# Optimization experiments

Hardware: AMD Instinct MI355X
Metric: run time of the kernel (lower is better)

## Reference

```python
import jax, jax.numpy as jnp
import numpy as np

EPS = 1e-5

def _layernorm(x, g, b):
    mu = jnp.mean(x, axis=-1, keepdims=True)
    var = jnp.mean(jnp.square(x - mu), axis=-1, keepdims=True)
    return (x - mu) / jnp.sqrt(var + EPS) * g + b

def setup_inputs() -> dict:
    key = jax.random.key(0)
    ks = jax.random.split(key, 8)
    B, T, E, H, Dh, F = 4, 2048, 1024, 16, 64, 4096
    s = lambda fan: 1.0 / np.sqrt(fan)
    return {
        "x":  jax.random.normal(ks[0], (B, T, E), jnp.float32),
        "Wq": jax.random.normal(ks[1], (H, E, Dh), jnp.float32) * s(E),
        "Wk": jax.random.normal(ks[2], (H, E, Dh), jnp.float32) * s(E),
        "Wv": jax.random.normal(ks[3], (H, E, Dh), jnp.float32) * s(E),
        "Wo": jax.random.normal(ks[4], (E, E), jnp.float32) * s(E),
        "bo": jnp.zeros((E,), jnp.float32),
        "W1": jax.random.normal(ks[5], (E, F), jnp.float32) * s(E),
        "b1": jnp.zeros((F,), jnp.float32),
        "W2": jax.random.normal(ks[6], (F, E), jnp.float32) * s(F),
        "b2": jnp.zeros((E,), jnp.float32),
        "g1": jnp.ones((E,), jnp.float32),
        "bt1": jnp.zeros((E,), jnp.float32),
        "g2": jnp.ones((E,), jnp.float32),
        "bt2": jnp.zeros((E,), jnp.float32),
    }

def reference(x, Wq, Wk, Wv, Wo, bo, W1, b1, W2, b2, g1, bt1, g2, bt2):
    B, T, E = x.shape
    # --- pre-LN multi-head attention (dropout = identity in eval) ---
    h = _layernorm(x, g1, bt1)
    q = jnp.einsum('btc,hcd->bhtd', h, Wq)
    k = jnp.einsum('btc,hcd->bhtd', h, Wk)
    v = jnp.einsum('btc,hcd->bhtd', h, Wv)
    # NOTE: original scales by embed_size**-0.5 (input channel c), not head_size
    scores = jnp.einsum('bhtd,bhsd->bhts', q, k) * (E ** -0.5)
    causal = jnp.tril(jnp.ones((T, T), bool))
    scores = jnp.where(causal, scores, -jnp.inf)
    attn = jax.nn.softmax(scores, axis=-1)
    ctx = jnp.einsum('bhts,bhsd->bhtd', attn, v)
    ctx = ctx.transpose(0, 2, 1, 3).reshape(B, T, E)  # concat heads
    x = x + ctx @ Wo + bo
    # --- pre-LN feed-forward ---
    h2 = _layernorm(x, g2, bt2)
    x = x + jax.nn.relu(h2 @ W1 + b1) @ W2 + b2
    return x
```

## Files before the change

kernel.cpp:

```cpp
#include <hip/hip_runtime.h>

typedef unsigned short u16;
typedef __attribute__((ext_vector_type(8))) short bf16x8;
typedef __attribute__((ext_vector_type(4))) short bf16x4;
typedef __attribute__((ext_vector_type(4))) float f32x4;

#define LOG2E 1.4426950408889634f

__device__ __forceinline__ float b2f(u16 u) {
  union { unsigned int i; float f; } x; x.i = ((unsigned int)u) << 16; return x.f;
}
__device__ __forceinline__ u16 f2b(float f) {
  unsigned int i = __float_as_uint(f);
  unsigned int r = (i + 0x7FFFu + ((i >> 16) & 1u)) >> 16;
  return (u16)r;
}
__device__ __forceinline__ void stc(u16* C, size_t i, float v) { C[i] = f2b(v); }
__device__ __forceinline__ void stc(float* C, size_t i, float v) { C[i] = v; }

__device__ __forceinline__ bool is_f32(const unsigned* probe) {
  return probe[0] == 0x3F800000u;
}
__device__ __forceinline__ float ldin(const void* p, size_t i, bool f32) {
  return f32 ? ((const float*)p)[i] : b2f(((const u16*)p)[i]);
}

__device__ __forceinline__ void gld_lds16(const void* g, void* l) {
  __builtin_amdgcn_global_load_lds(
      (const __attribute__((address_space(1))) unsigned int*)g,
      (__attribute__((address_space(3))) unsigned int*)l, 16, 0, 0);
}

__device__ __forceinline__ void lds_wave_fence() {
  __asm__ volatile("s_waitcnt lgkmcnt(0)" ::: "memory");
}

__device__ __forceinline__ void tr8(unsigned a[4], int lane) {
  unsigned p0, p1, p2, p3;
  p0 = __shfl_xor((int)a[0], 1, 64); p1 = __shfl_xor((int)a[1], 1, 64);
  p2 = __shfl_xor((int)a[2], 1, 64); p3 = __shfl_xor((int)a[3], 1, 64);
  unsigned sel = (lane & 1) ? 0x3276u : 0x5410u;
  a[0] = __byte_perm(a[0], p0, sel); a[1] = __byte_perm(a[1], p1, sel);
  a[2] = __byte_perm(a[2], p2, sel); a[3] = __byte_perm(a[3], p3, sel);
  p0 = __shfl_xor((int)a[0], 2, 64); p1 = __shfl_xor((int)a[1], 2, 64);
  p2 = __shfl_xor((int)a[2], 2, 64); p3 = __shfl_xor((int)a[3], 2, 64);
  if (lane & 2) { a[0] = p1; a[2] = p3; } else { a[1] = p0; a[3] = p2; }
  p0 = __shfl_xor((int)a[0], 4, 64); p1 = __shfl_xor((int)a[1], 4, 64);
  p2 = __shfl_xor((int)a[2], 4, 64); p3 = __shfl_xor((int)a[3], 4, 64);
  if (lane & 4) { a[0] = p2; a[1] = p3; } else { a[2] = p0; a[3] = p1; }
}

__global__ __launch_bounds__(256) void ln_kernel(
    const void* __restrict__ x, int x_raw,
    const void* __restrict__ g, const void* __restrict__ b,
    u16* __restrict__ y, const unsigned* __restrict__ probe) {
  __shared__ float red[4];
  const bool f32 = is_f32(probe);
  int row = blockIdx.x, tid = threadIdx.x;
  int w = tid >> 6;
  float f0, f1, f2, f3;
  if (x_raw && f32) {
    const float* xr = (const float*)x + (size_t)row * 1024 + tid * 4;
    float4 v = *(const float4*)xr;
    f0 = v.x; f1 = v.y; f2 = v.z; f3 = v.w;
  } else {
    const u16* xr = (const u16*)x + (size_t)row * 1024 + tid * 4;
    bf16x4 v = *(const bf16x4*)xr;
    f0 = b2f((u16)v[0]); f1 = b2f((u16)v[1]); f2 = b2f((u16)v[2]); f3 = b2f((u16)v[3]);
  }
  float s = f0 + f1 + f2 + f3;
  #pragma unroll
  for (int o = 32; o >= 1; o >>= 1) s += __shfl_xor(s, o, 64);
  if ((tid & 63) == 0) red[w] = s;
  __syncthreads();
  float mean = (red[0] + red[1] + red[2] + red[3]) * (1.0f / 1024.0f);
  __syncthreads();
  float d0 = f0 - mean, d1 = f1 - mean, d2 = f2 - mean, d3 = f3 - mean;
  float vs = d0 * d0 + d1 * d1 + d2 * d2 + d3 * d3;
  #pragma unroll
  for (int o = 32; o >= 1; o >>= 1) vs += __shfl_xor(vs, o, 64);
  if ((tid & 63) == 0) red[w] = vs;
  __syncthreads();
  float var = (red[0] + red[1] + red[2] + red[3]) * (1.0f / 1024.0f);
  float rstd = rsqrtf(var + 1e-5f);
  int c = tid * 4;
  float o0 = d0 * rstd * ldin(g, c + 0, f32) + ldin(b, c + 0, f32);
  float o1 = d1 * rstd * ldin(g, c + 1, f32) + ldin(b, c + 1, f32);
  float o2 = d2 * rstd * ldin(g, c + 2, f32) + ldin(b, c + 2, f32);
  float o3 = d3 * rstd * ldin(g, c + 3, f32) + ldin(b, c + 3, f32);
  bf16x4 ov; ov[0] = (short)f2b(o0); ov[1] = (short)f2b(o1);
  ov[2] = (short)f2b(o2); ov[3] = (short)f2b(o3);
  *(bf16x4*)(y + (size_t)row * 1024 + c) = ov;
}

__global__ __launch_bounds__(256) void repack_t(
    const void* __restrict__ src, u16* __restrict__ dst, int N, int K,
    const unsigned* __restrict__ probe) {
  const bool f32 = is_f32(probe);
  int flat = blockIdx.x * 256 + threadIdx.x;
  int n = flat % N;
  int c0 = (flat / N) * 8;
  bf16x8 t;
  #pragma unroll
  for (int j = 0; j < 8; j++) t[j] = (short)f2b(ldin(src, (size_t)(c0 + j) * N + n, f32));
  *(bf16x8*)&dst[(size_t)n * K + c0] = t;
}

__global__ __launch_bounds__(256) void repack_qkv(
    const void* __restrict__ Wq, const void* __restrict__ Wk,
    const void* __restrict__ Wv, u16* __restrict__ dst,
    const unsigned* __restrict__ probe) {
  const bool f32 = is_f32(probe);
  int flat = blockIdx.x * 256 + threadIdx.x;
  int n = flat % 3072;
  int c0 = (flat / 3072) * 8;
  const void* W = (n < 1024) ? Wq : (n < 2048) ? Wk : Wv;
  int nn = n & 1023;
  int hn = nn >> 6, d = nn & 63;
  bf16x8 t;
  #pragma unroll
  for (int j = 0; j < 8; j++)
    t[j] = (short)f2b(ldin(W, (size_t)hn * 65536 + (size_t)(c0 + j) * 64 + d, f32));
  *(bf16x8*)&dst[(size_t)n * 1024 + c0] = t;
}

template <int EPI, typename CT>
__global__ __launch_bounds__(256) void gemm_bt(
    const u16* __restrict__ A, const u16* __restrict__ Bt, CT* __restrict__ C,
    int M, int N, int K, const void* __restrict__ bias,
    const void* __restrict__ res, int res_raw,
    const unsigned* __restrict__ probe) {
  __shared__ __align__(16) u16 sA[128 * 32];
  __shared__ __align__(16) u16 sB[128 * 32];
  const bool f32 = is_f32(probe);
  int tid = threadIdx.x;
  int w = tid >> 6, lane = tid & 63;
  int l15 = lane & 15, q4 = lane >> 4;
  int bm = blockIdx.x * 128, bn = blockIdx.y * 128;
  int wm = (w & 1) * 64, wn = (w >> 1) * 64;
  f32x4 acc[4][4] = {};
  for (int k0 = 0; k0 < K; k0 += 32) {
    #pragma unroll
    for (int j = 0; j < 2; ++j) {
      int c = j * 256 + tid;
      int row = c >> 2, ck = (c & 3) * 8;
      gld_lds16(A + (size_t)(bm + row) * K + k0 + ck, &sA[c * 8]);
    }
    #pragma unroll
    for (int j = 0; j < 2; ++j) {
      int c = j * 256 + tid;
      int row = c >> 2, ck = (c & 3) * 8;
      gld_lds16(Bt + (size_t)(bn + row) * K + k0 + ck, &sB[c * 8]);
    }
    __syncthreads();
    bf16x8 af[4], bf[4];
    #pragma unroll
    for (int i = 0; i < 4; i++) af[i] = *(const bf16x8*)&sA[(wm + i * 16 + l15) * 32 + q4 * 8];
    #pragma unroll
    for (int j = 0; j < 4; j++) bf[j] = *(const bf16x8*)&sB[(wn + j * 16 + l15) * 32 + q4 * 8];
    #pragma unroll
    for (int i = 0; i < 4; i++)
      #pragma unroll
      for (int j = 0; j < 4; j++)
        acc[i][j] = __builtin_amdgcn_mfma_f32_16x16x32_bf16(af[i], bf[j], acc[i][j], 0, 0, 0);
    __syncthreads();
  }
  #pragma unroll
  for (int i = 0; i < 4; i++) {
    int rg = bm + wm + i * 16 + q4 * 4;
    #pragma unroll
    for (int j = 0; j < 4; j++) {
      int cg = bn + wn + j * 16 + l15;
      float bv = (EPI > 0) ? ldin(bias, cg, f32) : 0.0f;
      #pragma unroll
      for (int r = 0; r < 4; r++) {
        float v = acc[i][j][r];
        if (EPI == 1) v += bv + ldin(res, (size_t)(rg + r) * N + cg, res_raw && f32);
        if (EPI == 2) { v += bv; v = fmaxf(v, 0.0f); }
        stc(C, (size_t)(rg + r) * N + cg, v);
      }
    }
  }
}

__global__ __launch_bounds__(256) void attn_kernel(
    const u16* __restrict__ qkv, u16* __restrict__ ctx, int T) {
  __shared__ __align__(16) u16 sK[64 * 68];
  __shared__ __align__(16) u16 sVt[64 * 68];
  __shared__ __align__(16) u16 sP[8 * 16 * 68];
  int tid = threadIdx.x;
  int w = tid >> 6, lane = tid & 63;
  int l15 = lane & 15, q4 = lane >> 4;

  int n = blockIdx.x;
  int qi = n & 15;
  int h = (n >> 4) & 15;
  int b = (n >> 8) & 3;
  int qbase = (qi & 1) ? (qi >> 1) : (15 - (qi >> 1));
  int qt = (qbase + 7 * b) & 15;
  int qt0 = qt * 128;
  int mb[2] = {qt0 + w * 16, qt0 + 64 + w * 16};
  size_t b3072 = (size_t)(b * T) * 3072;

  bf16x8 qf[2][2];
  #pragma unroll
  for (int m = 0; m < 2; m++) {
    const u16* qr = qkv + b3072 + (size_t)(mb[m] + l15) * 3072 + h * 64;
    qf[m][0] = *(const bf16x8*)(qr + q4 * 8);
    qf[m][1] = *(const bf16x8*)(qr + 32 + q4 * 8);
  }
  f32x4 o[2][4] = {};
  float mx[2][4], ls[2][4];
  #pragma unroll
  for (int m = 0; m < 2; m++)
    #pragma unroll
    for (int r = 0; r < 4; r++) { mx[m][r] = -1e30f; ls[m][r] = 0.f; }

  int ktmax = 2 * qt + 1;
  for (int kt = 0; kt <= ktmax; ++kt) {
    int s0 = kt * 64;
    bf16x8 kreg[2]; int krow[2], kcol[2];
    #pragma unroll
    for (int j = 0; j < 2; ++j) {
      int c = j * 256 + tid;
      krow[j] = c >> 3; kcol[j] = (c & 7) * 8;
      kreg[j] = *(const bf16x8*)(qkv + b3072 + (size_t)(s0 + krow[j]) * 3072 + 1024 + h * 64 + kcol[j]);
    }
    unsigned va[4], vb[4];
    {
      const u16* vs = qkv + b3072 + (size_t)(s0 + lane) * 3072 + 2048 + h * 64 + w * 16;
      *(bf16x8*)va = *(const bf16x8*)vs;
      *(bf16x8*)vb = *(const bf16x8*)(vs + 8);
    }
    __syncthreads();
    #pragma unroll
    for (int j = 0; j < 2; ++j)
      *(bf16x8*)&sK[krow[j] * 68 + kcol[j]] = kreg[j];
    tr8(va, lane); tr8(vb, lane);
    {
      int dd = w * 16 + (lane & 7), t0 = (lane >> 3) * 8;
      *(bf16x8*)&sVt[dd * 68 + t0] = *(bf16x8*)va;
      *(bf16x8*)&sVt[(dd + 8) * 68 + t0] = *(bf16x8*)vb;
    }
    __syncthreads();

    bool act0 = (s0 <= mb[0] + 15);
    f32x4 s[2][4];
    #pragma unroll
    for (int j = 0; j < 4; ++j) {
      bf16x8 k0 = *(const bf16x8*)&sK[(j * 16 + l15) * 68 + q4 * 8];
      bf16x8 k1 = *(const bf16x8*)&sK[(j * 16 + l15) * 68 + 32 + q4 * 8];
      if (act0) {
        f32x4 z = {0.f, 0.f, 0.f, 0.f};
        z = __builtin_amdgcn_mfma_f32_16x16x32_bf16(qf[0][0], k0, z, 0, 0, 0);
        s[0][j] = __builtin_amdgcn_mfma_f32_16x16x32_bf16(qf[0][1], k1, z, 0, 0, 0);
      }
      f32x4 z = {0.f, 0.f, 0.f, 0.f};
      z = __builtin_amdgcn_mfma_f32_16x16x32_bf16(qf[1][0], k0, z, 0, 0, 0);
      s[1][j] = __builtin_amdgcn_mfma_f32_16x16x32_bf16(qf[1][1], k1, z, 0, 0, 0);
    }
    #pragma unroll
    for (int m = 0; m < 2; ++m) {
      if (m == 0 && !act0) continue;
      int mbm = mb[m];
      if (s0 + 63 > mbm) {
        #pragma unroll
        for (int j = 0; j < 4; ++j)
          #pragma unroll
          for (int r = 0; r < 4; ++r) {
            float v = s[m][j][r] * 0.03125f;
            if (s0 + j * 16 + l15 > mbm + q4 * 4 + r) v = -1e30f;
            s[m][j][r] = v;
          }
      } else {
        #pragma unroll
        for (int j = 0; j < 4; ++j)
          #pragma unroll
          for (int r = 0; r < 4; ++r) s[m][j][r] *= 0.03125f;
      }
      float tm[4];
      #pragma unroll
      for (int r = 0; r < 4; ++r)
        tm[r] = fmaxf(fmaxf(s[m][0][r], s[m][1][r]), fmaxf(s[m][2][r], s[m][3][r]));
      #pragma unroll
      for (int off = 8; off >= 1; off >>= 1)
        #pragma unroll
        for (int r = 0; r < 4; ++r) tm[r] = fmaxf(tm[r], __shfl_xor(tm[r], off, 64));
      float al[4], ts[4];
      #pragma unroll
      for (int r = 0; r < 4; ++r) {
        float mn = fmaxf(mx[m][r], tm[r]);
        al[r] = __builtin_amdgcn_exp2f((mx[m][r] - mn) * LOG2E);
        mx[m][r] = mn; ts[r] = 0.f;
      }
      int pbase = (w * 2 + m) * 1088;
      #pragma unroll
      for (int j = 0; j < 4; ++j)
        #pragma unroll
        for (int r = 0; r < 4; ++r) {
          float p = __builtin_amdgcn_exp2f((s[m][j][r] - mx[m][r]) * LOG2E);
          ts[r] += p;
          sP[pbase + (q4 * 4 + r) * 68 + j * 16 + l15] = f2b(p);
        }
      #pragma unroll
      for (int off = 8; off >= 1; off >>= 1)
        #pragma unroll
        for (int r = 0; r < 4; ++r) ts[r] += __shfl_xor(ts[r], off, 64);
      #pragma unroll
      for (int r = 0; r < 4; ++r) ls[m][r] = ls[m][r] * al[r] + ts[r];
      #pragma unroll
      for (int j = 0; j < 4; ++j)
        #pragma unroll
        for (int r = 0; r < 4; ++r) o[m][j][r] *= al[r];
    }
    lds_wave_fence();
    bf16x8 pf[2][2];
    #pragma unroll
    for (int m = 0; m < 2; ++m) {
      if (m == 0 && !act0) continue;
      int pbase = (w * 2 + m) * 1088;
      pf[m][0] = *(const bf16x8*)&sP[pbase + l15 * 68 + q4 * 8];
      pf[m][1] = *(const bf16x8*)&sP[pbase + l15 * 68 + 32 + q4 * 8];
    }
    #pragma unroll
    for (int j = 0; j < 4; ++j) {
      bf16x8 vf0 = *(const bf16x8*)&sVt[(j * 16 + l15) * 68 + q4 * 8];
      bf16x8 vf1 = *(const bf16x8*)&sVt[(j * 16 + l15) * 68 + 32 + q4 * 8];
      if (act0) {
        o[0][j] = __builtin_amdgcn_mfma_f32_16x16x32_bf16(pf[0][0], vf0, o[0][j], 0, 0, 0);
        o[0][j] = __builtin_amdgcn_mfma_f32_16x16x32_bf16(pf[0][1], vf1, o[0][j], 0, 0, 0);
      }
      o[1][j] = __builtin_amdgcn_mfma_f32_16x16x32_bf16(pf[1][0], vf0, o[1][j], 0, 0, 0);
      o[1][j] = __builtin_amdgcn_mfma_f32_16x16x32_bf16(pf[1][1], vf1, o[1][j], 0, 0, 0);
    }
  }
  #pragma unroll
  for (int m = 0; m < 2; ++m)
    #pragma unroll
    for (int j = 0; j < 4; ++j)
      #pragma unroll
      for (int r = 0; r < 4; ++r) {
        size_t addr = (size_t)(b * T + mb[m] + q4 * 4 + r) * 1024 + h * 64 + j * 16 + l15;
        ctx[addr] = f2b(o[m][j][r] / ls[m][r]);
      }
}

extern "C" void kernel_launch(void* const* d_in, const int* in_sizes, int n_in,
                              void* d_out, int out_size, void* d_ws, size_t ws_size,
                              hipStream_t stream) {
  (void)in_sizes; (void)n_in; (void)out_size; (void)ws_size;
  const void* x   = d_in[0];
  const void* Wq  = d_in[1];
  const void* Wk  = d_in[2];
  const void* Wv  = d_in[3];
  const void* Wo  = d_in[4];
  const void* bo  = d_in[5];
  const void* W1  = d_in[6];
  const void* b1  = d_in[7];
  const void* W2  = d_in[8];
  const void* b2  = d_in[9];
  const void* g1  = d_in[10];
  const void* bt1 = d_in[11];
  const void* g2  = d_in[12];
  const void* bt2 = d_in[13];
  const unsigned* probe = (const unsigned*)g1;
  float* out = (float*)d_out;

  const int BT = 8192, T = 2048;
  char* ws = (char*)d_ws;
  u16* hln    = (u16*)(ws);
  u16* qkv    = (u16*)(ws + 16777216);
  u16* ctx    = (u16*)(ws + 16777216 + 50331648);
  u16* a      = (u16*)(ws + 16777216);
  u16* x1     = (u16*)(ws + 83886080);
  u16* wqkv_t = (u16*)(ws + 100663296);
  u16* wo_t   = (u16*)(ws + 106954752);
  u16* w1_t   = (u16*)(ws + 109051904);
  u16* w2_t   = (u16*)(ws + 117440512);

  repack_qkv<<<1536, 256, 0, stream>>>(Wq, Wk, Wv, wqkv_t, probe);
  repack_t<<<512, 256, 0, stream>>>(Wo, wo_t, 1024, 1024, probe);
  repack_t<<<2048, 256, 0, stream>>>(W1, w1_t, 4096, 1024, probe);
  repack_t<<<2048, 256, 0, stream>>>(W2, w2_t, 1024, 4096, probe);

  ln_kernel<<<BT, 256, 0, stream>>>(x, 1, g1, bt1, hln, probe);
  gemm_bt<0, u16><<<dim3(64, 24), 256, 0, stream>>>(hln, wqkv_t, qkv, BT, 3072, 1024,
                                                    nullptr, nullptr, 0, probe);
  attn_kernel<<<1024, 256, 0, stream>>>(qkv, ctx, T);
  gemm_bt<1, u16><<<dim3(64, 8), 256, 0, stream>>>(ctx, wo_t, x1, BT, 1024, 1024,
                                                   bo, x, 1, probe);
  ln_kernel<<<BT, 256, 0, stream>>>(x1, 0, g2, bt2, hln, probe);
  gemm_bt<2, u16><<<dim3(64, 32), 256, 0, stream>>>(hln, w1_t, a, BT, 4096, 1024,
                                                    b1, nullptr, 0, probe);
  gemm_bt<1, float><<<dim3(64, 8), 256, 0, stream>>>(a, w2_t, out, BT, 1024, 4096,
                                                     b2, x1, 0, probe);
}
```

Baseline: 803.2 us.

## Pair causal query tiles per block and prefetch next K/V tile in attention

```diff
diff --git a/kernel.cpp b/kernel.cpp
--- a/kernel.cpp
+++ b/kernel.cpp
@@ -48,6 +48,16 @@
   p0 = __shfl_xor((int)a[0], 4, 64); p1 = __shfl_xor((int)a[1], 4, 64);
   p2 = __shfl_xor((int)a[2], 4, 64); p3 = __shfl_xor((int)a[3], 4, 64);
   if (lane & 4) { a[0] = p2; a[1] = p3; } else { a[2] = p0; a[3] = p1; }
+}
+
+struct KV { bf16x8 k0, k1; unsigned va[4], vb[4]; };
+__device__ __forceinline__ void load_kv(const u16* __restrict__ qkv, size_t b3072,
+                                        int h, int s0, int tid, int w, int lane, KV& t) {
+  t.k0 = *(const bf16x8*)(qkv + b3072 + (size_t)(s0 + (tid >> 3)) * 3072 + 1024 + h * 64 + (tid & 7) * 8);
+  t.k1 = *(const bf16x8*)(qkv + b3072 + (size_t)(s0 + 32 + (tid >> 3)) * 3072 + 1024 + h * 64 + (tid & 7) * 8);
+  const u16* vs = qkv + b3072 + (size_t)(s0 + lane) * 3072 + 2048 + h * 64 + w * 16;
+  *(bf16x8*)t.va = *(const bf16x8*)vs;
+  *(bf16x8*)t.vb = *(const bf16x8*)(vs + 8);
 }
 
 __global__ __launch_bounds__(256) void ln_kernel(
@@ -187,162 +197,151 @@
     const u16* __restrict__ qkv, u16* __restrict__ ctx, int T) {
   __shared__ __align__(16) u16 sK[64 * 68];
   __shared__ __align__(16) u16 sVt[64 * 68];
-  __shared__ __align__(16) u16 sP[8 * 16 * 68];
+  __shared__ __align__(16) u16 sP[4 * 16 * 68];
   int tid = threadIdx.x;
   int w = tid >> 6, lane = tid & 63;
   int l15 = lane & 15, q4 = lane >> 4;
-
   int n = blockIdx.x;
-  int qi = n & 15;
-  int h = (n >> 4) & 15;
-  int b = (n >> 8) & 3;
-  int qbase = (qi & 1) ? (qi >> 1) : (15 - (qi >> 1));
-  int qt = (qbase + 7 * b) & 15;
-  int qt0 = qt * 128;
-  int mb[2] = {qt0 + w * 16, qt0 + 64 + w * 16};
+  int qp = n & 7;
+  int h = (n >> 3) & 15;
+  int b = n >> 7;
   size_t b3072 = (size_t)(b * T) * 3072;
-
-  bf16x8 qf[2][2];
-  #pragma unroll
-  for (int m = 0; m < 2; m++) {
-    const u16* qr = qkv + b3072 + (size_t)(mb[m] + l15) * 3072 + h * 64;
-    qf[m][0] = *(const bf16x8*)(qr + q4 * 8);
-    qf[m][1] = *(const bf16x8*)(qr + 32 + q4 * 8);
+  int pbase = w * 1088;
+
+  for (int half = 0; half < 2; ++half) {
+    int qt = half ? (15 - qp) : qp;
+    int qt0 = qt * 128;
+    int mb0 = qt0 + w * 16, mb1 = qt0 + 64 + w * 16;
+    bf16x8 qf[2][2];
+    {
+      const u16* qr0 = qkv + b3072 + (size_t)(mb0 + l15) * 3072 + h * 64;
+      qf[0][0] = *(const bf16x8*)(qr0 + q4 * 8);
+      qf[0][1] = *(const bf16x8*)(qr0 + 32 + q4 * 8);
+      const u16* qr1 = qkv + b3072 + (size_t)(mb1 + l15) * 3072 + h * 64;
+      qf[1][0] = *(const bf16x8*)(qr1 + q4 * 8);
+      qf[1][1] = *(const bf16x8*)(qr1 + 32 + q4 * 8);
+    }
+    f32x4 o[2][4] = {};
+    float mx[2][4], ls[2][4];
+    #pragma unroll
+    for (int m = 0; m < 2; m++)
+      #pragma unroll
+      for (int r = 0; r < 4; r++) { mx[m][r] = -1e30f; ls[m][r] = 0.f; }
+
+    int L = 2 * qt + 2;
+    KV cur, nxt;
+    load_kv(qkv, b3072, h, 0, tid, w, lane, cur);
+    for (int kt = 0; kt < L; ++kt) {
+      int s0 = kt * 64;
+      __syncthreads();
+      *(bf16x8*)&sK[(tid >> 3) * 68 + (tid & 7) * 8] = cur.k0;
+      *(bf16x8*)&sK[(32 + (tid >> 3)) * 68 + (tid & 7) * 8] = cur.k1;
+      tr8(cur.va, lane); tr8(cur.vb, lane);
+      {
+        int dd = w * 16 + (lane & 7), t0 = (lane >> 3) * 8;
+        *(bf16x8*)&sVt[dd * 68 + t0] = *(bf16x8*)cur.va;
+        *(bf16x8*)&sVt[(dd + 8) * 68 + t0] = *(bf16x8*)cur.vb;
+      }
+      __syncthreads();
+      if (kt + 1 < L) load_kv(qkv, b3072, h, s0 + 64, tid, w, lane, nxt);
+
+      bool act0 = (s0 <= mb0 + 15);
+      f32x4 s[2][4];
+      #pragma unroll
+      for (int j = 0; j < 4; ++j) {
+        bf16x8 k0 = *(const bf16x8*)&sK[(j * 16 + l15) * 68 + q4 * 8];
+        bf16x8 k1 = *(const bf16x8*)&sK[(j * 16 + l15) * 68 + 32 + q4 * 8];
+        if (act0) {
+          f32x4 z = {0.f, 0.f, 0.f, 0.f};
+          z = __builtin_amdgcn_mfma_f32_16x16x32_bf16(qf[0][0], k0, z, 0, 0, 0);
+          s[0][j] = __builtin_amdgcn_mfma_f32_16x16x32_bf16(qf[0][1], k1, z, 0, 0, 0);
+        }
+        f32x4 z = {0.f, 0.f, 0.f, 0.f};
+        z = __builtin_amdgcn_mfma_f32_16x16x32_bf16(qf[1][0], k0, z, 0, 0, 0);
+        s[1][j] = __builtin_amdgcn_mfma_f32_16x16x32_bf16(qf[1][1], k1, z, 0, 0, 0);
+      }
+      bf16x8 pf[2][2];
+      #pragma unroll
+      for (int m = 0; m < 2; ++m) {
+        if (m == 0 && !act0) continue;
+        int mbm = m ? mb1 : mb0;
+        if (s0 + 63 > mbm) {
+          #pragma unroll
+          for (int j = 0; j < 4; ++j)
+            #pragma unroll
+            for (int r = 0; r < 4; ++r) {
+              float v = s[m][j][r] * 0.03125f;
+              if (s0 + j * 16 + l15 > mbm + q4 * 4 + r) v = -1e30f;
+              s[m][j][r] = v;
+            }
+        } else {
+          #pragma unroll
+          for (int j = 0; j < 4; ++j)
+            #pragma unroll
+            for (int r = 0; r < 4; ++r) s[m][j][r] *= 0.03125f;
+        }
+        float tm[4];
+        #pragma unroll
+        for (int r = 0; r < 4; ++r)
+          tm[r] = fmaxf(fmaxf(s[m][0][r], s[m][1][r]), fmaxf(s[m][2][r], s[m][3][r]));
+        #pragma unroll
+        for (int off = 8; off >= 1; off >>= 1)
+          #pragma unroll
+          for (int r = 0; r < 4; ++r) tm[r] = fmaxf(tm[r], __shfl_xor(tm[r], off, 64));
+        float al[4], ts[4];
+        #pragma unroll
+        for (int r = 0; r < 4; ++r) {
+          float mn = fmaxf(mx[m][r], tm[r]);
+          al[r] = __builtin_amdgcn_exp2f((mx[m][r] - mn) * LOG2E);
+          mx[m][r] = mn; ts[r] = 0.f;
+        }
+        #pragma unroll
+        for (int j = 0; j < 4; ++j)
+          #pragma unroll
+          for (int r = 0; r < 4; ++r) {
+            float p = __builtin_amdgcn_exp2f((s[m][j][r] - mx[m][r]) * LOG2E);
+            ts[r] += p;
+            sP[pbase + (q4 * 4 + r) * 68 + j * 16 + l15] = f2b(p);
+          }
+        #pragma unroll
+        for (int off = 8; off >= 1; off >>= 1)
+          #pragma unroll
+          for (int r = 0; r < 4; ++r) ts[r] += __shfl_xor(ts[r], off, 64);
+        #pragma unroll
+        for (int r = 0; r < 4; ++r) ls[m][r] = ls[m][r] * al[r] + ts[r];
+        #pragma unroll
+        for (int j = 0; j < 4; ++j)
+          #pragma unroll
+          for (int r = 0; r < 4; ++r) o[m][j][r] *= al[r];
+        lds_wave_fence();
+        pf[m][0] = *(const bf16x8*)&sP[pbase + l15 * 68 + q4 * 8];
+        pf[m][1] = *(const bf16x8*)&sP[pbase + l15 * 68 + 32 + q4 * 8];
+      }
+      #pragma unroll
+      for (int j = 0; j < 4; ++j) {
+        bf16x8 vf0 = *(const bf16x8*)&sVt[(j * 16 + l15) * 68 + q4 * 8];
+        bf16x8 vf1 = *(const bf16x8*)&sVt[(j * 16 + l15) * 68 + 32 + q4 * 8];
+        if (act0) {
+          o[0][j] = __builtin_amdgcn_mfma_f32_16x16x32_bf16(pf[0][0], vf0, o[0][j], 0, 0, 0);
+          o[0][j] = __builtin_amdgcn_mfma_f32_16x16x32_bf16(pf[0][1], vf1, o[0][j], 0, 0, 0);
+        }
+        o[1][j] = __builtin_amdgcn_mfma_f32_16x16x32_bf16(pf[1][0], vf0, o[1][j], 0, 0, 0);
+        o[1][j] = __builtin_amdgcn_mfma_f32_16x16x32_bf16(pf[1][1], vf1, o[1][j], 0, 0, 0);
+      }
+      if (kt + 1 < L) cur = nxt;
+    }
+    #pragma unroll
+    for (int m = 0; m < 2; ++m) {
+      int mbm = m ? mb1 : mb0;
+      #pragma unroll
+      for (int j = 0; j < 4; ++j)
+        #pragma unroll
+        for (int r = 0; r < 4; ++r) {
+          size_t addr = (size_t)(b * T + mbm + q4 * 4 + r) * 1024 + h * 64 + j * 16 + l15;
+          ctx[addr] = f2b(o[m][j][r] / ls[m][r]);
+        }
+    }
   }
-  f32x4 o[2][4] = {};
-  float mx[2][4], ls[2][4];
-  #pragma unroll
-  for (int m = 0; m < 2; m++)
-    #pragma unroll
-    for (int r = 0; r < 4; r++) { mx[m][r] = -1e30f; ls[m][r] = 0.f; }
-
-  int ktmax = 2 * qt + 1;
-  for (int kt = 0; kt <= ktmax; ++kt) {
-    int s0 = kt * 64;
-    bf16x8 kreg[2]; int krow[2], kcol[2];
-    #pragma unroll
-    for (int j = 0; j < 2; ++j) {
-      int c = j * 256 + tid;
-      krow[j] = c >> 3; kcol[j] = (c & 7) * 8;
-      kreg[j] = *(const bf16x8*)(qkv + b3072 + (size_t)(s0 + krow[j]) * 3072 + 1024 + h * 64 + kcol[j]);
-    }
-    unsigned va[4], vb[4];
-    {
-      const u16* vs = qkv + b3072 + (size_t)(s0 + lane) * 3072 + 2048 + h * 64 + w * 16;
-      *(bf16x8*)va = *(const bf16x8*)vs;
-      *(bf16x8*)vb = *(const bf16x8*)(vs + 8);
-    }
-    __syncthreads();
-    #pragma unroll
-    for (int j = 0; j < 2; ++j)
-      *(bf16x8*)&sK[krow[j] * 68 + kcol[j]] = kreg[j];
-    tr8(va, lane); tr8(vb, lane);
-    {
-      int dd = w * 16 + (lane & 7), t0 = (lane >> 3) * 8;
-      *(bf16x8*)&sVt[dd * 68 + t0] = *(bf16x8*)va;
-      *(bf16x8*)&sVt[(dd + 8) * 68 + t0] = *(bf16x8*)vb;
-    }
-    __syncthreads();
-
-    bool act0 = (s0 <= mb[0] + 15);
-    f32x4 s[2][4];
-    #pragma unroll
-    for (int j = 0; j < 4; ++j) {
-      bf16x8 k0 = *(const bf16x8*)&sK[(j * 16 + l15) * 68 + q4 * 8];
-      bf16x8 k1 = *(const bf16x8*)&sK[(j * 16 + l15) * 68 + 32 + q4 * 8];
-      if (act0) {
-        f32x4 z = {0.f, 0.f, 0.f, 0.f};
-        z = __builtin_amdgcn_mfma_f32_16x16x32_bf16(qf[0][0], k0, z, 0, 0, 0);
-        s[0][j] = __builtin_amdgcn_mfma_f32_16x16x32_bf16(qf[0][1], k1, z, 0, 0, 0);
-      }
-      f32x4 z = {0.f, 0.f, 0.f, 0.f};
-      z = __builtin_amdgcn_mfma_f32_16x16x32_bf16(qf[1][0], k0, z, 0, 0, 0);
-      s[1][j] = __builtin_amdgcn_mfma_f32_16x16x32_bf16(qf[1][1], k1, z, 0, 0, 0);
-    }
-    #pragma unroll
-    for (int m = 0; m < 2; ++m) {
-      if (m == 0 && !act0) continue;
-      int mbm = mb[m];
-      if (s0 + 63 > mbm) {
-        #pragma unroll
-        for (int j = 0; j < 4; ++j)
-          #pragma unroll
-          for (int r = 0; r < 4; ++r) {
-            float v = s[m][j][r] * 0.03125f;
-            if (s0 + j * 16 + l15 > mbm + q4 * 4 + r) v = -1e30f;
-            s[m][j][r] = v;
-          }
-      } else {
-        #pragma unroll
-        for (int j = 0; j < 4; ++j)
-          #pragma unroll
-          for (int r = 0; r < 4; ++r) s[m][j][r] *= 0.03125f;
-      }
-      float tm[4];
-      #pragma unroll
-      for (int r = 0; r < 4; ++r)
-        tm[r] = fmaxf(fmaxf(s[m][0][r], s[m][1][r]), fmaxf(s[m][2][r], s[m][3][r]));
-      #pragma unroll
-      for (int off = 8; off >= 1; off >>= 1)
-        #pragma unroll
-        for (int r = 0; r < 4; ++r) tm[r] = fmaxf(tm[r], __shfl_xor(tm[r], off, 64));
-      float al[4], ts[4];
-      #pragma unroll
-      for (int r = 0; r < 4; ++r) {
-        float mn = fmaxf(mx[m][r], tm[r]);
-        al[r] = __builtin_amdgcn_exp2f((mx[m][r] - mn) * LOG2E);
-        mx[m][r] = mn; ts[r] = 0.f;
-      }
-      int pbase = (w * 2 + m) * 1088;
-      #pragma unroll
-      for (int j = 0; j < 4; ++j)
-        #pragma unroll
-        for (int r = 0; r < 4; ++r) {
-          float p = __builtin_amdgcn_exp2f((s[m][j][r] - mx[m][r]) * LOG2E);
-          ts[r] += p;
-          sP[pbase + (q4 * 4 + r) * 68 + j * 16 + l15] = f2b(p);
-        }
-      #pragma unroll
-      for (int off = 8; off >= 1; off >>= 1)
-        #pragma unroll
-        for (int r = 0; r < 4; ++r) ts[r] += __shfl_xor(ts[r], off, 64);
-      #pragma unroll
-      for (int r = 0; r < 4; ++r) ls[m][r] = ls[m][r] * al[r] + ts[r];
-      #pragma unroll
-      for (int j = 0; j < 4; ++j)
-        #pragma unroll
-        for (int r = 0; r < 4; ++r) o[m][j][r] *= al[r];
-    }
-    lds_wave_fence();
-    bf16x8 pf[2][2];
-    #pragma unroll
-    for (int m = 0; m < 2; ++m) {
-      if (m == 0 && !act0) continue;
-      int pbase = (w * 2 + m) * 1088;
-      pf[m][0] = *(const bf16x8*)&sP[pbase + l15 * 68 + q4 * 8];
-      pf[m][1] = *(const bf16x8*)&sP[pbase + l15 * 68 + 32 + q4 * 8];
-    }
-    #pragma unroll
-    for (int j = 0; j < 4; ++j) {
-      bf16x8 vf0 = *(const bf16x8*)&sVt[(j * 16 + l15) * 68 + q4 * 8];
-      bf16x8 vf1 = *(const bf16x8*)&sVt[(j * 16 + l15) * 68 + 32 + q4 * 8];
-      if (act0) {
-        o[0][j] = __builtin_amdgcn_mfma_f32_16x16x32_bf16(pf[0][0], vf0, o[0][j], 0, 0, 0);
-        o[0][j] = __builtin_amdgcn_mfma_f32_16x16x32_bf16(pf[0][1], vf1, o[0][j], 0, 0, 0);
-      }
-      o[1][j] = __builtin_amdgcn_mfma_f32_16x16x32_bf16(pf[1][0], vf0, o[1][j], 0, 0, 0);
-      o[1][j] = __builtin_amdgcn_mfma_f32_16x16x32_bf16(pf[1][1], vf1, o[1][j], 0, 0, 0);
-    }
-  }
-  #pragma unroll
-  for (int m = 0; m < 2; ++m)
-    #pragma unroll
-    for (int j = 0; j < 4; ++j)
-      #pragma unroll
-      for (int r = 0; r < 4; ++r) {
-        size_t addr = (size_t)(b * T + mb[m] + q4 * 4 + r) * 1024 + h * 64 + j * 16 + l15;
-        ctx[addr] = f2b(o[m][j][r] / ls[m][r]);
-      }
 }
 
 extern "C" void kernel_launch(void* const* d_in, const int* in_sizes, int n_in,
@@ -386,7 +385,7 @@
   ln_kernel<<<BT, 256, 0, stream>>>(x, 1, g1, bt1, hln, probe);
   gemm_bt<0, u16><<<dim3(64, 24), 256, 0, stream>>>(hln, wqkv_t, qkv, BT, 3072, 1024,
                                                     nullptr, nullptr, 0, probe);
-  attn_kernel<<<1024, 256, 0, stream>>>(qkv, ctx, T);
+  attn_kernel<<<512, 256, 0, stream>>>(qkv, ctx, T);
   gemm_bt<1, u16><<<dim3(64, 8), 256, 0, stream>>>(ctx, wo_t, x1, BT, 1024, 1024,
                                                    bo, x, 1, probe);
   ln_kernel<<<BT, 256, 0, stream>>>(x1, 0, g2, bt2, hln, probe);
```

Result: faster. 690.3 us (-14.1%).
